# Kernel tuning notes

Measured on AMD Instinct MI355X. Metric: run time of the kernel, lower is better.

## Reference

```python
import jax, jax.numpy as jnp
import numpy as np

NUM_ROUTING = 3


def squash(s, axis):
    # v = |s|^2/(1+|s|^2) * s/|s|  (eq. 1 of the CapsNet paper)
    mag_sq = jnp.sum(s * s, axis=axis, keepdims=True)
    mag = jnp.sqrt(mag_sq)
    return mag_sq / (1.0 + mag_sq) * (s / mag)


def setup_inputs() -> dict:
    key = jax.random.key(0)
    k1, k2 = jax.random.split(key)
    B, I, C, U, S = 256, 8, 1152, 10, 16
    x = jax.random.normal(k1, (B, I, C), dtype=jnp.float32)
    weight = jax.random.normal(k2, (1, C, U, S, I), dtype=jnp.float32)
    return {"x": x, "weight": weight}


def reference(x, weight):
    # x: [B, in_unit, in_channel]; weight: [1, C, U, S, I]
    B = x.shape[0]
    C, U = weight.shape[1], weight.shape[2]
    x_t = jnp.transpose(x, (0, 2, 1))  # [B, C, I]
    # u_hat[b,c,u,s] = sum_i W[0,c,u,s,i] * x_t[b,c,i]
    u_hat = jnp.einsum('cusi,bci->bcus', weight[0], x_t)  # [B, C, U, S]

    b_ij = jnp.zeros((1, C, U, 1), dtype=u_hat.dtype)
    # s_j = (c_ij * u_hat).sum(dim=0): c_ij is batch-independent, so
    # precompute the batch-sum once instead of re-broadcasting each iter.
    u_sum = jnp.sum(u_hat, axis=0, keepdims=True)  # [1, C, U, S]

    v_j = None
    for _ in range(NUM_ROUTING):
        c_ij = jax.nn.softmax(b_ij, axis=2)          # [1, C, U, 1]
        s_j = c_ij * u_sum                           # [1, C, U, S]
        v_j = squash(s_j, axis=3)                    # [1, C, U, S]
        # agreement: mean over batch of <u_hat[b,c,u,:], v_j[0,c,u,:]>
        u_vj1 = jnp.einsum('bcus,cus->cu', u_hat, v_j[0]) / B  # [C, U]
        b_ij = b_ij + u_vj1[None, :, :, None]
    return v_j[0]  # squeeze -> [C, U, S]
```

## Files before the change

### kernel.cpp

```cpp
#include <hip/hip_runtime.h>

#define B_DIM 256
#define I_DIM 8
#define C_DIM 1152
#define U_DIM 10
#define S_DIM 16
#define ROWS  (B_DIM * I_DIM)
#define CPB   4
#define TPB   128

__global__ __launch_bounds__(TPB) void capsule_fused_kernel(
    const float* __restrict__ x, const float* __restrict__ W,
    float* __restrict__ out) {
    __shared__ float red[2][I_DIM][CPB];
    __shared__ float xs_lds[I_DIM][CPB];

    const int t = threadIdx.x;
    const int lane = t & 63;
    const int wv = t >> 6;
    const int c0 = blockIdx.x * CPB;

    float4 acc = make_float4(0.f, 0.f, 0.f, 0.f);
    const float* px = x + (size_t)t * C_DIM + c0;
#pragma unroll
    for (int k = 0; k < ROWS / TPB; ++k) {
        float4 v = *(const float4*)(px + (size_t)k * TPB * C_DIM);
        acc.x += v.x; acc.y += v.y; acc.z += v.z; acc.w += v.w;
    }
#pragma unroll
    for (int m = 8; m <= 32; m <<= 1) {
        acc.x += __shfl_xor(acc.x, m);
        acc.y += __shfl_xor(acc.y, m);
        acc.z += __shfl_xor(acc.z, m);
        acc.w += __shfl_xor(acc.w, m);
    }
    if (lane < I_DIM) {
        red[wv][lane][0] = acc.x; red[wv][lane][1] = acc.y;
        red[wv][lane][2] = acc.z; red[wv][lane][3] = acc.w;
    }
    __syncthreads();
    if (t < I_DIM * CPB) {
        const int i = t >> 2, col = t & 3;
        xs_lds[i][col] = red[0][i][col] + red[1][i][col];
    }
    __syncthreads();
    if (t >= 64) return;

    const int c_local = t >> 4;
    const int s = t & 15;
    const int c = c0 + c_local;

    float xs[I_DIM];
#pragma unroll
    for (int i = 0; i < I_DIM; ++i) xs[i] = xs_lds[i][c_local];

    float us[U_DIM];
#pragma unroll
    for (int u = 0; u < U_DIM; ++u) {
        const float4* w = (const float4*)(W + (((size_t)c * U_DIM + u) * S_DIM + s) * I_DIM);
        float4 w0 = w[0], w1 = w[1];
        us[u] = w0.x * xs[0] + w0.y * xs[1] + w0.z * xs[2] + w0.w * xs[3] +
                w1.x * xs[4] + w1.y * xs[5] + w1.z * xs[6] + w1.w * xs[7];
    }

    float bij[U_DIM];
    float v[U_DIM];

#pragma unroll
    for (int u = 0; u < U_DIM; ++u) {
        const float sj = 0.1f * us[u];
        float msq = sj * sj;
#pragma unroll
        for (int w = 1; w < 16; w <<= 1) msq += __shfl_xor(msq, w);
        const float mag = sqrtf(msq);
        const float v0 = (msq / (1.f + msq)) * (sj / mag);
        v[u] = v0;
        float a = us[u] * v0;
#pragma unroll
        for (int w = 1; w < 16; w <<= 1) a += __shfl_xor(a, w);
        bij[u] = a * (1.f / (float)B_DIM);
    }

#pragma unroll
    for (int it = 1; it < 3; ++it) {
        float m = bij[0];
#pragma unroll
        for (int u = 1; u < U_DIM; ++u) m = fmaxf(m, bij[u]);
        float e[U_DIM];
        float sum = 0.f;
#pragma unroll
        for (int u = 0; u < U_DIM; ++u) { e[u] = __expf(bij[u] - m); sum += e[u]; }
        const float inv = 1.f / sum;

#pragma unroll
        for (int u = 0; u < U_DIM; ++u) {
            const float sj = e[u] * inv * us[u];
            float msq = sj * sj;
#pragma unroll
            for (int w = 1; w < 16; w <<= 1) msq += __shfl_xor(msq, w);
            const float mag = sqrtf(msq);
            const float vv = (msq / (1.f + msq)) * (sj / mag);
            v[u] = vv;
            if (it < 2) {
                float a = us[u] * vv;
#pragma unroll
                for (int w = 1; w < 16; w <<= 1) a += __shfl_xor(a, w);
                bij[u] += a * (1.f / (float)B_DIM);
            }
        }
    }

#pragma unroll
    for (int u = 0; u < U_DIM; ++u)
        out[(size_t)c * (U_DIM * S_DIM) + u * S_DIM + s] = v[u];
}

extern "C" void kernel_launch(void* const* d_in, const int* in_sizes, int n_in,
                              void* d_out, int out_size, void* d_ws, size_t ws_size,
                              hipStream_t stream) {
    const float* x = (const float*)d_in[0];
    const float* W = (const float*)d_in[1];
    float* out = (float*)d_out;

    capsule_fused_kernel<<<C_DIM / CPB, TPB, 0, stream>>>(x, W, out);
}
```

Measured before the change: 81.08 us.

## Process 16 capsules per block with 256 threads and full-row float4 loads

```diff
diff --git a/kernel.cpp b/kernel.cpp
--- a/kernel.cpp
+++ b/kernel.cpp
@@ -6,45 +6,49 @@
 #define U_DIM 10
 #define S_DIM 16
 #define ROWS  (B_DIM * I_DIM)
-#define CPB   4
-#define TPB   128
+#define CPB   16
+#define TPB   256
 
 __global__ __launch_bounds__(TPB) void capsule_fused_kernel(
     const float* __restrict__ x, const float* __restrict__ W,
     float* __restrict__ out) {
-    __shared__ float red[2][I_DIM][CPB];
-    __shared__ float xs_lds[I_DIM][CPB];
+    __shared__ float4 red4[4][I_DIM][4];
+    __shared__ float  xs_lds[I_DIM][CPB];
 
     const int t = threadIdx.x;
     const int lane = t & 63;
     const int wv = t >> 6;
     const int c0 = blockIdx.x * CPB;
 
-    float4 acc = make_float4(0.f, 0.f, 0.f, 0.f);
-    const float* px = x + (size_t)t * C_DIM + c0;
+    {
+        const int rgrp = t >> 2;
+        const int chunk = t & 3;
+        const float* px = x + (size_t)rgrp * C_DIM + c0 + 4 * chunk;
+        float4 acc = make_float4(0.f, 0.f, 0.f, 0.f);
 #pragma unroll
-    for (int k = 0; k < ROWS / TPB; ++k) {
-        float4 v = *(const float4*)(px + (size_t)k * TPB * C_DIM);
-        acc.x += v.x; acc.y += v.y; acc.z += v.z; acc.w += v.w;
-    }
-#pragma unroll
-    for (int m = 8; m <= 32; m <<= 1) {
-        acc.x += __shfl_xor(acc.x, m);
-        acc.y += __shfl_xor(acc.y, m);
-        acc.z += __shfl_xor(acc.z, m);
-        acc.w += __shfl_xor(acc.w, m);
-    }
-    if (lane < I_DIM) {
-        red[wv][lane][0] = acc.x; red[wv][lane][1] = acc.y;
-        red[wv][lane][2] = acc.z; red[wv][lane][3] = acc.w;
+        for (int k = 0; k < ROWS / 64; ++k) {
+            float4 v = *(const float4*)(px + (size_t)k * 64 * C_DIM);
+            acc.x += v.x; acc.y += v.y; acc.z += v.z; acc.w += v.w;
+        }
+        acc.x += __shfl_xor(acc.x, 32);
+        acc.y += __shfl_xor(acc.y, 32);
+        acc.z += __shfl_xor(acc.z, 32);
+        acc.w += __shfl_xor(acc.w, 32);
+        if (lane < 32)
+            red4[wv][lane >> 2][lane & 3] = acc;
     }
     __syncthreads();
-    if (t < I_DIM * CPB) {
-        const int i = t >> 2, col = t & 3;
-        xs_lds[i][col] = red[0][i][col] + red[1][i][col];
+    if (t < 32) {
+        const int i = t >> 2, chunk = t & 3;
+        float4 a0 = red4[0][i][chunk], a1 = red4[1][i][chunk];
+        float4 a2 = red4[2][i][chunk], a3 = red4[3][i][chunk];
+        float4 sum = make_float4(a0.x + a1.x + a2.x + a3.x,
+                                 a0.y + a1.y + a2.y + a3.y,
+                                 a0.z + a1.z + a2.z + a3.z,
+                                 a0.w + a1.w + a2.w + a3.w);
+        *(float4*)&xs_lds[i][chunk * 4] = sum;
     }
     __syncthreads();
-    if (t >= 64) return;
 
     const int c_local = t >> 4;
     const int s = t & 15;
```

Result: faster. 73.21 us (-9.7%).
